# Performance work log

Hardware: AMD Instinct MI355X
Metric: run time of the kernel (lower is better)

The kernel has to match this reference:

```python
import jax, jax.numpy as jnp
import numpy as np

TOP_K = 2
NORM_TOPK_PROB = True


def setup_inputs() -> dict:
    key = jax.random.key(0)
    k1, k2, k3, k4 = jax.random.split(key, 4)
    B, S, H = 1, 1024, 2048
    E, I = 16, 768
    hidden_states = jax.random.normal(k1, (B, S, H), dtype=jnp.float32)
    # 0.02 init scale keeps router logits / activations in a realistic range
    gate_w = jax.random.normal(k2, (E, H), dtype=jnp.float32) * 0.02
    w1 = jax.random.normal(k3, (E, 2 * I, H), dtype=jnp.float32) * 0.02  # [gate; up] stacked
    w2 = jax.random.normal(k4, (E, H, I), dtype=jnp.float32) * 0.02
    return {"hidden_states": hidden_states, "gate_w": gate_w, "w1": w1, "w2": w2}


def reference(hidden_states, gate_w, w1, w2):
    B, S, H = hidden_states.shape
    E = gate_w.shape[0]
    I = w2.shape[2]
    x = hidden_states.reshape(-1, H)  # [T, H]

    # Router
    router_logits = x @ gate_w.T  # [T, E]
    probs = jax.nn.softmax(router_logits.astype(jnp.float32), axis=-1)
    topk_w, topk_ids = jax.lax.top_k(probs, TOP_K)  # [T, K]
    if NORM_TOPK_PROB:
        topk_w = topk_w / jnp.sum(topk_w, axis=-1, keepdims=True)
    topk_w = topk_w.astype(x.dtype)

    # combine[t, e] = sum_k topk_w[t, k] * 1[topk_ids[t, k] == e]
    combine = jnp.sum(jax.nn.one_hot(topk_ids, E, dtype=x.dtype) * topk_w[..., None], axis=1)  # [T, E]

    def expert(w1_e, w2_e):
        h = x @ w1_e.T                      # [T, 2I]
        act = jax.nn.silu(h[:, :I]) * h[:, I:]  # fused SiLU-and-mul
        return act @ w2_e.T                 # [T, H]

    y_all = jax.vmap(expert)(w1, w2)        # [E, T, H]
    out = jnp.einsum('te,eth->th', combine, y_all)  # weighted scatter-sum over experts
    return out, router_logits
```

## Files before the change

kernel.cpp:

```cpp
#include <hip/hip_runtime.h>
#include <hip/hip_bf16.h>


#define T_TOK 1024
#define HDIM  2048
#define NEXP  16
#define IDIM  768
#define CAP   192

typedef __attribute__((ext_vector_type(8))) short  short8_t;
typedef __attribute__((ext_vector_type(4))) float  f32x4_t;

static __device__ __forceinline__ unsigned short f2bf(float f) {
  unsigned u = __float_as_uint(f);
  u += 0x7FFFu + ((u >> 16) & 1u);
  return (unsigned short)(u >> 16);
}
static __device__ __forceinline__ short f2bf_t(float f) {
  return (short)(__float_as_uint(f) >> 16);
}
static __device__ __forceinline__ float bf2f(unsigned short h) {
  return __uint_as_float(((unsigned)h) << 16);
}
static __device__ __forceinline__ short8_t pack_bf16(float4 lo, float4 hi) {
  short8_t r;
  r[0] = f2bf_t(lo.x); r[1] = f2bf_t(lo.y); r[2] = f2bf_t(lo.z); r[3] = f2bf_t(lo.w);
  r[4] = f2bf_t(hi.x); r[5] = f2bf_t(hi.y); r[6] = f2bf_t(hi.z); r[7] = f2bf_t(hi.w);
  return r;
}
static __device__ __forceinline__ short8_t pack8_rne(float4 lo, float4 hi) {
  short8_t r;
  r[0] = (short)f2bf(lo.x); r[1] = (short)f2bf(lo.y);
  r[2] = (short)f2bf(lo.z); r[3] = (short)f2bf(lo.w);
  r[4] = (short)f2bf(hi.x); r[5] = (short)f2bf(hi.y);
  r[6] = (short)f2bf(hi.z); r[7] = (short)f2bf(hi.w);
  return r;
}
static __device__ __forceinline__ void gl2lds16(const void* g, void* l) {
  __builtin_amdgcn_global_load_lds(
      (const __attribute__((address_space(1))) unsigned int*)g,
      (__attribute__((address_space(3))) unsigned int*)l, 16, 0, 0);
}

__global__ __launch_bounds__(256) void moe_router(
    const float* __restrict__ x, const float* __restrict__ gw,
    float* __restrict__ logits_out, int* __restrict__ cnt,
    int* __restrict__ tok, int* __restrict__ inv, float* __restrict__ invw,
    unsigned short* __restrict__ xb) {
  const int t = blockIdx.x;
  const int tid = threadIdx.x;
  const int lane = tid & 63, wid = tid >> 6;
  const float4* xv = (const float4*)(x + (size_t)t * HDIM);
  float4 v0 = xv[tid * 2], v1 = xv[tid * 2 + 1];
  *(short8_t*)(xb + (size_t)t * HDIM + tid * 8) = pack8_rne(v0, v1);
  float acc[NEXP];
#pragma unroll
  for (int e = 0; e < NEXP; ++e) {
    const float4* gv = (const float4*)(gw + (size_t)e * HDIM);
    float4 g0 = gv[tid * 2], g1 = gv[tid * 2 + 1];
    acc[e] = v0.x * g0.x + v0.y * g0.y + v0.z * g0.z + v0.w * g0.w +
             v1.x * g1.x + v1.y * g1.y + v1.z * g1.z + v1.w * g1.w;
  }
#pragma unroll
  for (int e = 0; e < NEXP; ++e)
#pragma unroll
    for (int off = 32; off; off >>= 1) acc[e] += __shfl_xor(acc[e], off, 64);
  __shared__ float red[4][NEXP];
  if (lane == 0)
#pragma unroll
    for (int e = 0; e < NEXP; ++e) red[wid][e] = acc[e];
  __syncthreads();
  if (tid < NEXP) {
    float s = red[0][tid] + red[1][tid] + red[2][tid] + red[3][tid];
    logits_out[(size_t)t * NEXP + tid] = s;
    red[0][tid] = s;
  }
  __syncthreads();
  if (tid == 0) {
    int e1 = -1, e2 = -1;
    float l1 = -1e30f, l2 = -1e30f;
#pragma unroll
    for (int e = 0; e < NEXP; ++e) {
      float v = red[0][e];
      if (v > l1)      { l2 = l1; e2 = e1; l1 = v; e1 = e; }
      else if (v > l2) { l2 = v;  e2 = e; }
    }
    float wa = 1.f / (1.f + __expf(l2 - l1));
    float wb = 1.f - wa;
    int p1 = atomicAdd(&cnt[e1], 1);
    int i0 = 0; float w0 = 0.f;
    if (p1 < CAP) { tok[e1 * CAP + p1] = t; i0 = e1 * CAP + p1; w0 = wa; }
    inv[t * 2] = i0; invw[t * 2] = w0;
    int p2 = atomicAdd(&cnt[e2], 1);
    int i1 = 0; float w1 = 0.f;
    if (p2 < CAP) { tok[e2 * CAP + p2] = t; i1 = e2 * CAP + p2; w1 = wb; }
    inv[t * 2 + 1] = i1; invw[t * 2 + 1] = w1;
  }
}

__global__ __launch_bounds__(256) void moe_stage_a(
    const unsigned short* __restrict__ xb, const float* __restrict__ w1,
    const int* __restrict__ cnt, const int* __restrict__ tok,
    unsigned short* __restrict__ h_ws) {
  int bx = blockIdx.x;
  bx = (bx & 7) * 96 + (bx >> 3);
  const int ks = bx & 1;
  const int nt = (bx >> 1) % 24;
  const int e  = (bx >> 1) / 24;
  int ne = cnt[e]; if (ne > CAP) ne = CAP;

  __shared__ unsigned short As[2][192 * 32];
  __shared__ float          Bs[2][64 * 32];
  __shared__ int toksL[192];
  const int tid = threadIdx.x;
  if (tid < 192)
    toksL[tid] = tok[e * CAP + (tid < ne ? tid : (ne ? ne - 1 : 0))] & (T_TOK - 1);
  __syncthreads();

  const int w = tid >> 6, lane = tid & 63;
  const int k0 = ks * 1024;

  const unsigned short* aG[3];
  int aOff[3];
#pragma unroll
  for (int jj = 0; jj < 3; ++jj) {
    int j = w * 3 + jj;
    int row = 16 * j + (lane >> 2);
    aG[jj] = xb + (size_t)toksL[row] * HDIM + k0 + (lane & 3) * 8;
    aOff[jj] = j * 512;
  }
  const float* bG[2];
  int bOff[2];
#pragma unroll
  for (int jj = 0; jj < 2; ++jj) {
    int j = w * 2 + jj;
    int nrow = 8 * j + (lane >> 3);
    int d = ((lane & 7) - (lane >> 3)) & 7;
    bG[jj] = w1 + ((size_t)e * (2 * IDIM) + nt * 64 + nrow) * HDIM + k0 + d * 4;
    bOff[jj] = j * 256;
  }

  const int quad = lane >> 4, lr = lane & 15;
  f32x4_t acc[3][4] = {};

#pragma unroll
  for (int jj = 0; jj < 3; ++jj) gl2lds16(aG[jj], &As[0][aOff[jj]]);
#pragma unroll
  for (int jj = 0; jj < 2; ++jj) gl2lds16(bG[jj], &Bs[0][bOff[jj]]);

  for (int it = 0; it < 32; ++it) {
    const int cur = it & 1;
    if (it < 31) {
      const int kk = (it + 1) * 32;
#pragma unroll
      for (int jj = 0; jj < 3; ++jj) gl2lds16(aG[jj] + kk, &As[cur ^ 1][aOff[jj]]);
#pragma unroll
      for (int jj = 0; jj < 2; ++jj) gl2lds16(bG[jj] + kk, &Bs[cur ^ 1][bOff[jj]]);
      asm volatile("s_waitcnt vmcnt(5)" ::: "memory");
    } else {
      asm volatile("s_waitcnt vmcnt(0)" ::: "memory");
    }
    __builtin_amdgcn_s_barrier();
    __builtin_amdgcn_sched_barrier(0);

    short8_t a[3], b[4];
#pragma unroll
    for (int mf = 0; mf < 3; ++mf) {
      int row = w * 48 + mf * 16 + lr;
      a[mf] = *(const short8_t*)&As[cur][row * 32 + quad * 8];
    }
#pragma unroll
    for (int nf = 0; nf < 4; ++nf) {
      int r = nf * 16 + lr;
      int p0 = (2 * quad + r) & 7, p1 = (2 * quad + 1 + r) & 7;
      float4 f0 = *(const float4*)&Bs[cur][r * 32 + p0 * 4];
      float4 f1 = *(const float4*)&Bs[cur][r * 32 + p1 * 4];
      b[nf] = pack_bf16(f0, f1);
    }
#pragma unroll
    for (int mf = 0; mf < 3; ++mf)
#pragma unroll
      for (int nf = 0; nf < 4; ++nf)
        acc[mf][nf] = __builtin_amdgcn_mfma_f32_16x16x32_bf16(
            a[mf], b[nf], acc[mf][nf], 0, 0, 0);
    asm volatile("s_waitcnt lgkmcnt(0)" ::: "memory");
    __builtin_amdgcn_s_barrier();
    __builtin_amdgcn_sched_barrier(0);
  }

  unsigned short* hp = h_ws + ((size_t)ks * NEXP + e) * CAP * (2 * IDIM);
#pragma unroll
  for (int mf = 0; mf < 3; ++mf) {
#pragma unroll
    for (int rr = 0; rr < 4; ++rr) {
      int mg = w * 48 + mf * 16 + quad * 4 + rr;
#pragma unroll
      for (int nf = 0; nf < 4; ++nf) {
        int ng = nt * 64 + nf * 16 + lr;
        hp[(size_t)mg * (2 * IDIM) + ng] = f2bf(acc[mf][nf][rr]);
      }
    }
  }
}

__global__ __launch_bounds__(256) void moe_merge(
    const unsigned short* __restrict__ h_ws, unsigned short* __restrict__ act) {
  const size_t part = (size_t)NEXP * CAP * (2 * IDIM);
  int c = blockIdx.x * 256 + threadIdx.x;
  int row = c / (IDIM / 4);
  int c4  = c % (IDIM / 4);
  size_t gb = (size_t)row * (2 * IDIM) + c4 * 4;
  ushort4 g0 = *(const ushort4*)(h_ws + gb);
  ushort4 g1 = *(const ushort4*)(h_ws + part + gb);
  ushort4 u0 = *(const ushort4*)(h_ws + gb + IDIM);
  ushort4 u1 = *(const ushort4*)(h_ws + part + gb + IDIM);
  float g, u; ushort4 o;
  g = bf2f(g0.x) + bf2f(g1.x); u = bf2f(u0.x) + bf2f(u1.x);
  o.x = f2bf(g / (1.f + __expf(-g)) * u);
  g = bf2f(g0.y) + bf2f(g1.y); u = bf2f(u0.y) + bf2f(u1.y);
  o.y = f2bf(g / (1.f + __expf(-g)) * u);
  g = bf2f(g0.z) + bf2f(g1.z); u = bf2f(u0.z) + bf2f(u1.z);
  o.z = f2bf(g / (1.f + __expf(-g)) * u);
  g = bf2f(g0.w) + bf2f(g1.w); u = bf2f(u0.w) + bf2f(u1.w);
  o.w = f2bf(g / (1.f + __expf(-g)) * u);
  *(ushort4*)(act + (size_t)row * IDIM + c4 * 4) = o;
}

__global__ __launch_bounds__(256) void moe_stage_b(
    const unsigned short* __restrict__ act, const float* __restrict__ w2,
    float* __restrict__ y) {
  int bx = blockIdx.x;
  bx = (bx & 7) * 64 + (bx >> 3);
  const int nt = bx & 31;
  const int e  = bx >> 5;

  __shared__ unsigned short As[2][192 * 32];
  __shared__ float          Bs[2][64 * 32];
  const int tid = threadIdx.x;
  const int w = tid >> 6, lane = tid & 63;

  const unsigned short* aG[3];
  int aOff[3];
#pragma unroll
  for (int jj = 0; jj < 3; ++jj) {
    int j = w * 3 + jj;
    int slot = 16 * j + (lane >> 2);
    aG[jj] = act + ((size_t)e * CAP + slot) * IDIM + (lane & 3) * 8;
    aOff[jj] = j * 512;
  }
  const float* bG[2];
  int bOff[2];
#pragma unroll
  for (int jj = 0; jj < 2; ++jj) {
    int j = w * 2 + jj;
    int nrow = 8 * j + (lane >> 3);
    int d = ((lane & 7) - (lane >> 3)) & 7;
    bG[jj] = w2 + ((size_t)e * HDIM + nt * 64 + nrow) * IDIM + d * 4;
    bOff[jj] = j * 256;
  }

  const int quad = lane >> 4, lr = lane & 15;
  f32x4_t acc[3][4] = {};

#pragma unroll
  for (int jj = 0; jj < 3; ++jj) gl2lds16(aG[jj], &As[0][aOff[jj]]);
#pragma unroll
  for (int jj = 0; jj < 2; ++jj) gl2lds16(bG[jj], &Bs[0][bOff[jj]]);

  for (int it = 0; it < 24; ++it) {
    const int cur = it & 1;
    if (it < 23) {
      const int kk = (it + 1) * 32;
#pragma unroll
      for (int jj = 0; jj < 3; ++jj) gl2lds16(aG[jj] + kk, &As[cur ^ 1][aOff[jj]]);
#pragma unroll
      for (int jj = 0; jj < 2; ++jj) gl2lds16(bG[jj] + kk, &Bs[cur ^ 1][bOff[jj]]);
      asm volatile("s_waitcnt vmcnt(5)" ::: "memory");
    } else {
      asm volatile("s_waitcnt vmcnt(0)" ::: "memory");
    }
    __builtin_amdgcn_s_barrier();
    __builtin_amdgcn_sched_barrier(0);

    short8_t a[3], b[4];
#pragma unroll
    for (int mf = 0; mf < 3; ++mf) {
      int row = w * 48 + mf * 16 + lr;
      a[mf] = *(const short8_t*)&As[cur][row * 32 + quad * 8];
    }
#pragma unroll
    for (int nf = 0; nf < 4; ++nf) {
      int r = nf * 16 + lr;
      int p0 = (2 * quad + r) & 7, p1 = (2 * quad + 1 + r) & 7;
      float4 f0 = *(const float4*)&Bs[cur][r * 32 + p0 * 4];
      float4 f1 = *(const float4*)&Bs[cur][r * 32 + p1 * 4];
      b[nf] = pack_bf16(f0, f1);
    }
#pragma unroll
    for (int mf = 0; mf < 3; ++mf)
#pragma unroll
      for (int nf = 0; nf < 4; ++nf)
        acc[mf][nf] = __builtin_amdgcn_mfma_f32_16x16x32_bf16(
            a[mf], b[nf], acc[mf][nf], 0, 0, 0);
    asm volatile("s_waitcnt lgkmcnt(0)" ::: "memory");
    __builtin_amdgcn_s_barrier();
    __builtin_amdgcn_sched_barrier(0);
  }

#pragma unroll
  for (int mf = 0; mf < 3; ++mf) {
#pragma unroll
    for (int rr = 0; rr < 4; ++rr) {
      int sl = w * 48 + mf * 16 + quad * 4 + rr;
#pragma unroll
      for (int nf = 0; nf < 4; ++nf) {
        int ng = nt * 64 + nf * 16 + lr;
        y[((size_t)e * CAP + sl) * HDIM + ng] = acc[mf][nf][rr];
      }
    }
  }
}

__global__ __launch_bounds__(256) void moe_combine(
    const float* __restrict__ y, const int* __restrict__ inv,
    const float* __restrict__ invw, float* __restrict__ out) {
  const int t = blockIdx.x;
  const int i0 = inv[t * 2], i1 = inv[t * 2 + 1];
  const float w0 = invw[t * 2], w1 = invw[t * 2 + 1];
  const float4* y0 = (const float4*)(y + (size_t)i0 * HDIM);
  const float4* y1 = (const float4*)(y + (size_t)i1 * HDIM);
  float4* op = (float4*)(out + (size_t)t * HDIM);
#pragma unroll
  for (int rep = 0; rep < 2; ++rep) {
    int c = threadIdx.x + rep * 256;
    float4 a = y0[c], b = y1[c];
    float4 r;
    r.x = w0 * a.x + w1 * b.x;
    r.y = w0 * a.y + w1 * b.y;
    r.z = w0 * a.z + w1 * b.z;
    r.w = w0 * a.w + w1 * b.w;
    op[c] = r;
  }
}

extern "C" void kernel_launch(void* const* d_in, const int* in_sizes, int n_in,
                              void* d_out, int out_size, void* d_ws,
                              size_t ws_size, hipStream_t stream) {
  (void)in_sizes; (void)n_in; (void)out_size; (void)ws_size;
  const float* x  = (const float*)d_in[0];
  const float* gw = (const float*)d_in[1];
  const float* w1 = (const float*)d_in[2];
  const float* w2 = (const float*)d_in[3];
  float* out    = (float*)d_out;
  float* logits = out + (size_t)T_TOK * HDIM;

  char* ws = (char*)d_ws;
  int*   cnt  = (int*)ws;
  int*   tok  = (int*)(ws + 256);
  int*   inv  = (int*)(ws + 12544);
  float* invw = (float*)(ws + 20736);
  unsigned short* xb  = (unsigned short*)(ws + 28928);
  unsigned short* act = xb;
  unsigned short* h_ws = (unsigned short*)(ws + 4747520);
  float*          yb   = (float*)(ws + 23621888);

  hipMemsetAsync(cnt, 0, 256, stream);

  moe_router <<<T_TOK, 256, 0, stream>>>(x, gw, logits, cnt, tok, inv, invw, xb);
  moe_stage_a<<<NEXP * 24 * 2, 256, 0, stream>>>(xb, w1, cnt, tok, h_ws);
  moe_merge  <<<NEXP * CAP * IDIM / 4 / 256, 256, 0, stream>>>(h_ws, act);
  moe_stage_b<<<NEXP * 32, 256, 0, stream>>>(act, w2, yb);
  moe_combine<<<T_TOK, 256, 0, stream>>>(yb, inv, invw, out);
}
```

Measured before the change: 430.6 us.

## Convert fp32 weight tiles to bf16 once per block in LDS, swizzle A tile

Both expert GEMM kernels now load the fp32 weight tile into registers, pack it to bf16 once per thread and store it to a padded bf16 LDS tile. This replaces the earlier scheme where each wave read the fp32 tile from LDS and converted it redundantly. The A-tile load columns are XOR-swizzled and read back with a matching swizzle to avoid LDS bank conflicts. The cost is an extra register-staged global load path with its own prefetch and an additional barrier/lgkm wait per k-step.

```diff
diff --git a/kernel.cpp b/kernel.cpp
--- a/kernel.cpp
+++ b/kernel.cpp
@@ -41,6 +41,42 @@
       (const __attribute__((address_space(1))) unsigned int*)g,
       (__attribute__((address_space(3))) unsigned int*)l, 16, 0, 0);
 }
+
+#define GEMM_STEP(NSTEP, t, CUR, RC0, RC1, RN0, RN1)                         \
+  {                                                                          \
+    if ((t) + 1 < (NSTEP)) {                                                 \
+      const int kk_ = ((t) + 1) * 32;                                        \
+      gl2lds16(aG[0] + kk_, &As[(CUR) ^ 1][aOff[0]]);                        \
+      gl2lds16(aG[1] + kk_, &As[(CUR) ^ 1][aOff[1]]);                        \
+      gl2lds16(aG[2] + kk_, &As[(CUR) ^ 1][aOff[2]]);                        \
+      RN0 = *(const float4*)(bG + kk_);                                      \
+      RN1 = *(const float4*)(bG + kk_ + 4);                                  \
+      asm volatile("s_waitcnt vmcnt(5)" ::: "memory");                       \
+    } else {                                                                 \
+      asm volatile("s_waitcnt vmcnt(0)" ::: "memory");                       \
+    }                                                                        \
+    __builtin_amdgcn_sched_barrier(0);                                       \
+    *(short8_t*)&Bs[CUR][bOff] = pack_bf16(RC0, RC1);                        \
+    asm volatile("s_waitcnt lgkmcnt(0)" ::: "memory");                       \
+    __builtin_amdgcn_s_barrier();                                            \
+    __builtin_amdgcn_sched_barrier(0);                                       \
+    short8_t a_[3], b_[4];                                                   \
+    _Pragma("unroll") for (int mf = 0; mf < 3; ++mf) {                       \
+      int row_ = w * 48 + mf * 16 + lr;                                      \
+      a_[mf] = *(const short8_t*)&As[CUR][row_ * 32 + (quad ^ axor) * 8];    \
+    }                                                                        \
+    _Pragma("unroll") for (int nf = 0; nf < 4; ++nf) {                       \
+      int r_ = nf * 16 + lr;                                                 \
+      b_[nf] = *(const short8_t*)&Bs[CUR][r_ * 40 + quad * 8];               \
+    }                                                                        \
+    _Pragma("unroll") for (int mf = 0; mf < 3; ++mf)                         \
+      _Pragma("unroll") for (int nf = 0; nf < 4; ++nf)                       \
+        acc[mf][nf] = __builtin_amdgcn_mfma_f32_16x16x32_bf16(               \
+            a_[mf], b_[nf], acc[mf][nf], 0, 0, 0);                           \
+    asm volatile("s_waitcnt lgkmcnt(0)" ::: "memory");                       \
+    __builtin_amdgcn_s_barrier();                                            \
+    __builtin_amdgcn_sched_barrier(0);                                       \
+  }
 
 __global__ __launch_bounds__(256) void moe_router(
     const float* __restrict__ x, const float* __restrict__ gw,
@@ -110,7 +146,7 @@
   int ne = cnt[e]; if (ne > CAP) ne = CAP;
 
   __shared__ unsigned short As[2][192 * 32];
-  __shared__ float          Bs[2][64 * 32];
+  __shared__ unsigned short Bs[2][64 * 40];
   __shared__ int toksL[192];
   const int tid = threadIdx.x;
   if (tid < 192)
@@ -119,6 +155,8 @@
 
   const int w = tid >> 6, lane = tid & 63;
   const int k0 = ks * 1024;
+  const int quad = lane >> 4, lr = lane & 15;
+  const int axor = (lr >> 1) & 3;
 
   const unsigned short* aG[3];
   int aOff[3];
@@ -126,66 +164,26 @@
   for (int jj = 0; jj < 3; ++jj) {
     int j = w * 3 + jj;
     int row = 16 * j + (lane >> 2);
-    aG[jj] = xb + (size_t)toksL[row] * HDIM + k0 + (lane & 3) * 8;
+    int cdat = (lane & 3) ^ ((lane >> 3) & 3);
+    aG[jj] = xb + (size_t)toksL[row] * HDIM + k0 + cdat * 8;
     aOff[jj] = j * 512;
   }
-  const float* bG[2];
-  int bOff[2];
-#pragma unroll
-  for (int jj = 0; jj < 2; ++jj) {
-    int j = w * 2 + jj;
-    int nrow = 8 * j + (lane >> 3);
-    int d = ((lane & 7) - (lane >> 3)) & 7;
-    bG[jj] = w1 + ((size_t)e * (2 * IDIM) + nt * 64 + nrow) * HDIM + k0 + d * 4;
-    bOff[jj] = j * 256;
-  }
-
-  const int quad = lane >> 4, lr = lane & 15;
+  const int br = tid >> 2, bc = tid & 3;
+  const float* bG = w1 + ((size_t)e * (2 * IDIM) + nt * 64 + br) * HDIM + k0 + bc * 8;
+  const int bOff = br * 40 + bc * 8;
+
   f32x4_t acc[3][4] = {};
 
-#pragma unroll
-  for (int jj = 0; jj < 3; ++jj) gl2lds16(aG[jj], &As[0][aOff[jj]]);
-#pragma unroll
-  for (int jj = 0; jj < 2; ++jj) gl2lds16(bG[jj], &Bs[0][bOff[jj]]);
-
-  for (int it = 0; it < 32; ++it) {
-    const int cur = it & 1;
-    if (it < 31) {
-      const int kk = (it + 1) * 32;
-#pragma unroll
-      for (int jj = 0; jj < 3; ++jj) gl2lds16(aG[jj] + kk, &As[cur ^ 1][aOff[jj]]);
-#pragma unroll
-      for (int jj = 0; jj < 2; ++jj) gl2lds16(bG[jj] + kk, &Bs[cur ^ 1][bOff[jj]]);
-      asm volatile("s_waitcnt vmcnt(5)" ::: "memory");
-    } else {
-      asm volatile("s_waitcnt vmcnt(0)" ::: "memory");
-    }
-    __builtin_amdgcn_s_barrier();
-    __builtin_amdgcn_sched_barrier(0);
-
-    short8_t a[3], b[4];
-#pragma unroll
-    for (int mf = 0; mf < 3; ++mf) {
-      int row = w * 48 + mf * 16 + lr;
-      a[mf] = *(const short8_t*)&As[cur][row * 32 + quad * 8];
-    }
-#pragma unroll
-    for (int nf = 0; nf < 4; ++nf) {
-      int r = nf * 16 + lr;
-      int p0 = (2 * quad + r) & 7, p1 = (2 * quad + 1 + r) & 7;
-      float4 f0 = *(const float4*)&Bs[cur][r * 32 + p0 * 4];
-      float4 f1 = *(const float4*)&Bs[cur][r * 32 + p1 * 4];
-      b[nf] = pack_bf16(f0, f1);
-    }
-#pragma unroll
-    for (int mf = 0; mf < 3; ++mf)
-#pragma unroll
-      for (int nf = 0; nf < 4; ++nf)
-        acc[mf][nf] = __builtin_amdgcn_mfma_f32_16x16x32_bf16(
-            a[mf], b[nf], acc[mf][nf], 0, 0, 0);
-    asm volatile("s_waitcnt lgkmcnt(0)" ::: "memory");
-    __builtin_amdgcn_s_barrier();
-    __builtin_amdgcn_sched_barrier(0);
+  gl2lds16(aG[0], &As[0][aOff[0]]);
+  gl2lds16(aG[1], &As[0][aOff[1]]);
+  gl2lds16(aG[2], &As[0][aOff[2]]);
+  float4 p0 = *(const float4*)(bG);
+  float4 p1 = *(const float4*)(bG + 4);
+  float4 q0 = {}, q1 = {};
+
+  for (int it2 = 0; it2 < 16; ++it2) {
+    GEMM_STEP(32, it2 * 2,     0, p0, p1, q0, q1);
+    GEMM_STEP(32, it2 * 2 + 1, 1, q0, q1, p0, p1);
   }
 
   unsigned short* hp = h_ws + ((size_t)ks * NEXP + e) * CAP * (2 * IDIM);
@@ -235,9 +233,11 @@
   const int e  = bx >> 5;
 
   __shared__ unsigned short As[2][192 * 32];
-  __shared__ float          Bs[2][64 * 32];
+  __shared__ unsigned short Bs[2][64 * 40];
   const int tid = threadIdx.x;
   const int w = tid >> 6, lane = tid & 63;
+  const int quad = lane >> 4, lr = lane & 15;
+  const int axor = (lr >> 1) & 3;
 
   const unsigned short* aG[3];
   int aOff[3];
@@ -245,66 +245,26 @@
   for (int jj = 0; jj < 3; ++jj) {
     int j = w * 3 + jj;
     int slot = 16 * j + (lane >> 2);
-    aG[jj] = act + ((size_t)e * CAP + slot) * IDIM + (lane & 3) * 8;
+    int cdat = (lane & 3) ^ ((lane >> 3) & 3);
+    aG[jj] = act + ((size_t)e * CAP + slot) * IDIM + cdat * 8;
     aOff[jj] = j * 512;
   }
-  const float* bG[2];
-  int bOff[2];
-#pragma unroll
-  for (int jj = 0; jj < 2; ++jj) {
-    int j = w * 2 + jj;
-    int nrow = 8 * j + (lane >> 3);
-    int d = ((lane & 7) - (lane >> 3)) & 7;
-    bG[jj] = w2 + ((size_t)e * HDIM + nt * 64 + nrow) * IDIM + d * 4;
-    bOff[jj] = j * 256;
-  }
-
-  const int quad = lane >> 4, lr = lane & 15;
+  const int br = tid >> 2, bc = tid & 3;
+  const float* bG = w2 + ((size_t)e * HDIM + nt * 64 + br) * IDIM + bc * 8;
+  const int bOff = br * 40 + bc * 8;
+
   f32x4_t acc[3][4] = {};
 
-#pragma unroll
-  for (int jj = 0; jj < 3; ++jj) gl2lds16(aG[jj], &As[0][aOff[jj]]);
-#pragma unroll
-  for (int jj = 0; jj < 2; ++jj) gl2lds16(bG[jj], &Bs[0][bOff[jj]]);
-
-  for (int it = 0; it < 24; ++it) {
-    const int cur = it & 1;
-    if (it < 23) {
-      const int kk = (it + 1) * 32;
-#pragma unroll
-      for (int jj = 0; jj < 3; ++jj) gl2lds16(aG[jj] + kk, &As[cur ^ 1][aOff[jj]]);
-#pragma unroll
-      for (int jj = 0; jj < 2; ++jj) gl2lds16(bG[jj] + kk, &Bs[cur ^ 1][bOff[jj]]);
-      asm volatile("s_waitcnt vmcnt(5)" ::: "memory");
-    } else {
-      asm volatile("s_waitcnt vmcnt(0)" ::: "memory");
-    }
-    __builtin_amdgcn_s_barrier();
-    __builtin_amdgcn_sched_barrier(0);
-
-    short8_t a[3], b[4];
-#pragma unroll
-    for (int mf = 0; mf < 3; ++mf) {
-      int row = w * 48 + mf * 16 + lr;
-      a[mf] = *(const short8_t*)&As[cur][row * 32 + quad * 8];
-    }
-#pragma unroll
-    for (int nf = 0; nf < 4; ++nf) {
-      int r = nf * 16 + lr;
-      int p0 = (2 * quad + r) & 7, p1 = (2 * quad + 1 + r) & 7;
-      float4 f0 = *(const float4*)&Bs[cur][r * 32 + p0 * 4];
-      float4 f1 = *(const float4*)&Bs[cur][r * 32 + p1 * 4];
-      b[nf] = pack_bf16(f0, f1);
-    }
-#pragma unroll
-    for (int mf = 0; mf < 3; ++mf)
-#pragma unroll
-      for (int nf = 0; nf < 4; ++nf)
-        acc[mf][nf] = __builtin_amdgcn_mfma_f32_16x16x32_bf16(
-            a[mf], b[nf], acc[mf][nf], 0, 0, 0);
-    asm volatile("s_waitcnt lgkmcnt(0)" ::: "memory");
-    __builtin_amdgcn_s_barrier();
-    __builtin_amdgcn_sched_barrier(0);
+  gl2lds16(aG[0], &As[0][aOff[0]]);
+  gl2lds16(aG[1], &As[0][aOff[1]]);
+  gl2lds16(aG[2], &As[0][aOff[2]]);
+  float4 p0 = *(const float4*)(bG);
+  float4 p1 = *(const float4*)(bG + 4);
+  float4 q0 = {}, q1 = {};
+
+  for (int it2 = 0; it2 < 12; ++it2) {
+    GEMM_STEP(24, it2 * 2,     0, p0, p1, q0, q1);
+    GEMM_STEP(24, it2 * 2 + 1, 1, q0, q1, p0, p1);
   }
 
 #pragma unroll
```

After: 412.0 us. 4.3% less time.
